# Performance work log

Measured on AMD Instinct MI355X. Metric: run time of the kernel, lower is better.

## Reference

```python
import jax, jax.numpy as jnp
import numpy as np

B_SZ, L, D_MODEL = 2, 2048, 2048
INTER, HEADS, P, N, G, K = 4096, 64, 64, 128, 1, 4
CONV_DIM = INTER + 2 * G * N
EPS = 1e-5


def silu(x):
    return x * jax.nn.sigmoid(x)


def softplus_thresh(x, threshold=10.0):
    # matches source: where(x < thr, log(1+exp(x)), x)
    return jnp.where(x < threshold, jnp.log1p(jnp.exp(jnp.minimum(x, threshold))), x)


def setup_inputs() -> dict:
    key = jax.random.key(0)
    ks = jax.random.split(key, 8)
    s = 0.02
    return {
        "hidden_states": jax.random.normal(ks[0], (B_SZ, L, D_MODEL), jnp.float32),
        "W_z": jax.random.normal(ks[1], (D_MODEL, INTER), jnp.float32) * s,
        "W_xBC": jax.random.normal(ks[2], (D_MODEL, CONV_DIM), jnp.float32) * s,
        "W_dt": jax.random.normal(ks[3], (D_MODEL, HEADS), jnp.float32) * s,
        "conv_w": jax.random.normal(ks[4], (CONV_DIM, K), jnp.float32) * 0.1,
        "conv_b": jnp.zeros((CONV_DIM,), jnp.float32),
        "dt_bias": jax.random.uniform(ks[5], (HEADS,), jnp.float32, -2.0, 0.0),
        "A_log": jnp.log(jnp.arange(1, HEADS + 1, dtype=jnp.float32)),
        "D": jnp.ones((HEADS,), jnp.float32),
        "norm_w": jnp.ones((INTER,), jnp.float32),
        "W_out": jax.random.normal(ks[6], (INTER, D_MODEL), jnp.float32) * s,
    }


def reference(hidden_states, W_z, W_xBC, W_dt, conv_w, conv_b, dt_bias, A_log, D, norm_w, W_out):
    b, l, _ = hidden_states.shape
    Hg = HEADS // G  # heads per group

    gate = hidden_states @ W_z                      # [b,l,INTER]
    xBC = hidden_states @ W_xBC                     # [b,l,CONV_DIM]
    dt = softplus_thresh(hidden_states @ W_dt + dt_bias)  # [b,l,H]

    # causal depthwise conv1d + silu (padding=K-1, truncated to seq_len)
    xp = jnp.pad(xBC, ((0, 0), (K - 1, 0), (0, 0)))
    kern = jnp.transpose(conv_w)[:, None, :]        # [K,1,CONV_DIM] (WIO)
    xBC = jax.lax.conv_general_dilated(
        xp, kern, (1,), 'VALID',
        dimension_numbers=('NWC', 'WIO', 'NWC'),
        feature_group_count=CONV_DIM)
    xBC = silu(xBC + conv_b)

    gns = G * N
    x = xBC[..., :INTER].reshape(b, l, G, Hg, P)
    Bm = xBC[..., INTER:INTER + gns].reshape(b, l, G, N)
    Cm = xBC[..., INTER + gns:].reshape(b, l, G, N)

    A = -jnp.exp(A_log)                             # [H]
    dA = jnp.exp(dt * A).reshape(b, l, G, Hg)       # [b,l,G,Hg]
    dtx = dt.reshape(b, l, G, Hg)[..., None] * x    # [b,l,G,Hg,P]

    def step(state, inp):
        dA_t, dtx_t, B_t, C_t = inp
        # state: [b,G,Hg,P,N]
        state = state * dA_t[..., None, None] + dtx_t[..., None] * B_t[:, :, None, None, :]
        y_t = jnp.einsum('bghpn,bgn->bghp', state, C_t)
        return state, y_t

    xs = (jnp.moveaxis(dA, 1, 0), jnp.moveaxis(dtx, 1, 0),
          jnp.moveaxis(Bm, 1, 0), jnp.moveaxis(Cm, 1, 0))
    state0 = jnp.zeros((b, G, Hg, P, N), jnp.float32)
    _, ys = jax.lax.scan(step, state0, xs)          # [l,b,G,Hg,P]
    y = jnp.moveaxis(ys, 0, 1) + D.reshape(G, Hg)[..., None] * x
    scan_out = y.reshape(b, l, INTER)

    # gated RMSNorm within groups
    hs = scan_out.reshape(b, l, G, INTER // G).astype(jnp.float32)
    gt = gate.reshape(b, l, G, INTER // G).astype(jnp.float32)
    hs = hs * silu(gt)
    var = jnp.mean(hs * hs, axis=-1, keepdims=True)
    hs = hs * jax.lax.rsqrt(var + EPS)
    normed = norm_w * hs.reshape(b, l, INTER)

    return normed @ W_out
```

## Files before the change

kernel.cpp:

```cpp
#include <hip/hip_runtime.h>
#include <hip/hip_bf16.h>
#include <math.h>

typedef unsigned short u16;
typedef unsigned int   u32;
typedef __attribute__((ext_vector_type(8))) short short8;
typedef __attribute__((ext_vector_type(4))) float f32x4;

#define B_SZ     2
#define LSEQ     2048
#define DMODEL   2048
#define INTER    4096
#define HEADS    64
#define NSTATE   128
#define CONV_DIM 4352
#define XCOLS    4480
#define EPS      1e-5f
#define QCH      64
#define NCHUNK   (LSEQ / QCH)

__device__ __forceinline__ float bf2f(u16 u) {
    u32 v = ((u32)u) << 16;
    return __builtin_bit_cast(float, v);
}
__device__ __forceinline__ u16 f2bf(float x) {
    __hip_bfloat16 h = __float2bfloat16(x);
    return __builtin_bit_cast(u16, h);
}
__device__ __forceinline__ u32 pack2(float lo, float hi) {
    return (u32)f2bf(lo) | ((u32)f2bf(hi) << 16);
}
__device__ __forceinline__ void gl2lds16(const void* g, void* l) {
    __builtin_amdgcn_global_load_lds(
        (const __attribute__((address_space(1))) u32*)g,
        (__attribute__((address_space(3))) u32*)l, 16, 0, 0);
}

__global__ __launch_bounds__(256) void cvt_f32_bf16(
    const float* __restrict__ in, u16* __restrict__ out, int n4)
{
    int i = blockIdx.x * 256 + threadIdx.x;
    if (i >= n4) return;
    float4 v = ((const float4*)in)[i];
    ushort4 o;
    o.x = f2bf(v.x); o.y = f2bf(v.y); o.z = f2bf(v.z); o.w = f2bf(v.w);
    ((ushort4*)out)[i] = o;
}

__global__ __launch_bounds__(256) void tr_f32_bf16(
    const float* __restrict__ in, u16* __restrict__ out, int R, int C)
{
    __shared__ u16 tile[64][68];
    const int r0 = blockIdx.y * 64, c0 = blockIdx.x * 64;
    const int tr = threadIdx.x >> 4, tc = (threadIdx.x & 15) * 4;
    #pragma unroll
    for (int i = 0; i < 4; ++i) {
        int r = tr + i * 16;
        float4 v = *(const float4*)(in + (size_t)(r0 + r) * C + c0 + tc);
        tile[r][tc + 0] = f2bf(v.x);
        tile[r][tc + 1] = f2bf(v.y);
        tile[r][tc + 2] = f2bf(v.z);
        tile[r][tc + 3] = f2bf(v.w);
    }
    __syncthreads();
    #pragma unroll
    for (int i = 0; i < 4; ++i) {
        int oc = tr + i * 16;
        ushort4 o;
        o.x = tile[tc + 0][oc];
        o.y = tile[tc + 1][oc];
        o.z = tile[tc + 2][oc];
        o.w = tile[tc + 3][oc];
        *(ushort4*)(out + (size_t)(c0 + oc) * R + r0 + tc) = o;
    }
}

template<int OUT_BF16>
__global__ __launch_bounds__(256) void gemm_nt(
    const u16* __restrict__ A, const u16* __restrict__ Bt,
    void* __restrict__ Co, int M, int N, int K)
{
    __shared__ __align__(16) u16 As[128 * 32];
    __shared__ __align__(16) u16 Bs[128 * 32];
    const int tid  = threadIdx.x;
    const int wave = tid >> 6, lane = tid & 63;
    const int m0 = blockIdx.y * 128, n0 = blockIdx.x * 128;
    const int wm = (wave >> 1) * 64, wn = (wave & 1) * 64;

    const int srow = wave * 16 + (lane >> 2);
    const int scol = (lane & 3) * 8;
    const u16* ag = A  + (size_t)(m0 + srow) * K + scol;
    const u16* bg = Bt + (size_t)(n0 + srow) * K + scol;
    u16* asl = As + wave * (16 * 32);
    u16* bsl = Bs + wave * (16 * 32);

    f32x4 acc[4][4];
    #pragma unroll
    for (int i = 0; i < 4; ++i)
        #pragma unroll
        for (int j = 0; j < 4; ++j) acc[i][j] = (f32x4)0.f;

    const int lr = lane & 15, lq = lane >> 4;
    const u16* arp = As + (wm + lr) * 32 + lq * 8;
    const u16* brp = Bs + (wn + lr) * 32 + lq * 8;

    for (int k0 = 0; k0 < K; k0 += 32) {
        __syncthreads();
        gl2lds16(ag + k0,          asl);
        gl2lds16(ag + 64 * K + k0, asl + 64 * 32);
        gl2lds16(bg + k0,          bsl);
        gl2lds16(bg + 64 * K + k0, bsl + 64 * 32);
        __syncthreads();

        short8 af[4], bfr[4];
        #pragma unroll
        for (int i = 0; i < 4; ++i) af[i]  = *(const short8*)(arp + i * 16 * 32);
        #pragma unroll
        for (int j = 0; j < 4; ++j) bfr[j] = *(const short8*)(brp + j * 16 * 32);
        #pragma unroll
        for (int i = 0; i < 4; ++i)
            #pragma unroll
            for (int j = 0; j < 4; ++j)
                acc[i][j] = __builtin_amdgcn_mfma_f32_16x16x32_bf16(
                    af[i], bfr[j], acc[i][j], 0, 0, 0);
    }

    #pragma unroll
    for (int i = 0; i < 4; ++i)
        #pragma unroll
        for (int j = 0; j < 4; ++j)
            #pragma unroll
            for (int r = 0; r < 4; ++r) {
                int row = m0 + wm + i * 16 + lq * 4 + r;
                int col = n0 + wn + j * 16 + lr;
                if (OUT_BF16)
                    ((u16*)Co)[(size_t)row * N + col] = f2bf(acc[i][j][r]);
                else
                    ((float*)Co)[(size_t)row * N + col] = acc[i][j][r];
            }
}

__global__ void dt_kernel(const u16* __restrict__ xpre,
                          float* __restrict__ dtb,
                          const float* __restrict__ dt_bias, int n)
{
    int i = blockIdx.x * 256 + threadIdx.x;
    if (i >= n) return;
    int h = i & 63, row = i >> 6;
    float x = bf2f(xpre[(size_t)row * XCOLS + CONV_DIM + h]) + dt_bias[h];
    dtb[i] = (x < 10.f) ? log1pf(expf(x)) : x;
}

__global__ void conv_kernel(const u16* __restrict__ xin,
                            const float* __restrict__ cw,
                            const float* __restrict__ cb,
                            u16* __restrict__ xout)
{
    int c  = blockIdx.x * 256 + threadIdx.x;
    int bt = blockIdx.y;
    int t  = bt & (LSEQ - 1);
    const u16* xi = xin + (size_t)bt * XCOLS + c;
    float4 w = *(const float4*)(cw + (size_t)c * 4);
    float acc = cb[c];
    acc = fmaf(bf2f(xi[0]), w.w, acc);
    if (t >= 1) acc = fmaf(bf2f(*(xi - XCOLS)),     w.z, acc);
    if (t >= 2) acc = fmaf(bf2f(*(xi - 2 * XCOLS)), w.y, acc);
    if (t >= 3) acc = fmaf(bf2f(*(xi - 3 * XCOLS)), w.x, acc);
    xout[(size_t)bt * CONV_DIM + c] = f2bf(acc / (1.f + expf(-acc)));
}

__global__ __launch_bounds__(256) void ssd_chunk_state(
    const u16* __restrict__ xc, const float* __restrict__ dtb,
    const float* __restrict__ A_log,
    u16* __restrict__ Tg, float* __restrict__ decayQ)
{
    const int bid = blockIdx.x;
    const int b = bid >> 11, h = (bid >> 5) & 63, c = bid & 31;
    const int t0 = c * QCH;
    const int tid = threadIdx.x;
    const int wave = tid >> 6, lane = tid & 63;
    const int lr = lane & 15, lq = lane >> 4;

    __shared__ __align__(16) u16 BT[128][72];
    __shared__ __align__(16) u16 XwT[64][72];
    __shared__ float sclL[QCH];

    const u16* xg = xc + (size_t)b * LSEQ * CONV_DIM;

    if (tid < 64) {
        float dtv = dtb[((size_t)b * LSEQ + t0 + tid) * HEADS + h];
        float a = -dtv * expf(A_log[h]);
        float s = a;
        #pragma unroll
        for (int off = 1; off < 64; off <<= 1) {
            float o = __shfl_up(s, off, 64);
            if (tid >= off) s += o;
        }
        float cq = __shfl(s, 63, 64);
        sclL[tid] = dtv * expf(cq - s);
        if (tid == 0) decayQ[((b * 64 + h) << 5) + c] = expf(cq);
    }
    __syncthreads();

    #pragma unroll
    for (int r = 0; r < 16; ++r) {
        int idx = tid + 256 * r, j = idx >> 6, p = idx & 63;
        float v = bf2f(xg[(size_t)(t0 + j) * CONV_DIM + h * 64 + p]);
        XwT[p][j] = f2bf(v * sclL[j]);
    }
    #pragma unroll
    for (int r = 0; r < 32; ++r) {
        int idx = tid + 256 * r, j = idx >> 7, n = idx & 127;
        BT[n][j] = xg[(size_t)(t0 + j) * CONV_DIM + INTER + n];
    }
    __syncthreads();

    f32x4 acc[8];
    #pragma unroll
    for (int i = 0; i < 8; ++i) acc[i] = (f32x4)0.f;
    #pragma unroll
    for (int k0 = 0; k0 < QCH; k0 += 32) {
        short8 af = *(const short8*)&XwT[wave * 16 + lr][k0 + lq * 8];
        #pragma unroll
        for (int nt = 0; nt < 8; ++nt) {
            short8 bfr = *(const short8*)&BT[nt * 16 + lr][k0 + lq * 8];
            acc[nt] = __builtin_amdgcn_mfma_f32_16x16x32_bf16(af, bfr, acc[nt], 0, 0, 0);
        }
    }
    u16* To = Tg + ((((size_t)(b * 64 + h)) * NCHUNK + c) * 64) * 128;
    #pragma unroll
    for (int nt = 0; nt < 8; ++nt)
        #pragma unroll
        for (int r = 0; r < 4; ++r)
            To[(wave * 16 + lq * 4 + r) * 128 + nt * 16 + lr] = f2bf(acc[nt][r]);
}

__global__ __launch_bounds__(256) void ssd_state_scan(
    u16* __restrict__ Tg, const float* __restrict__ decayQ)
{
    const int bh = blockIdx.x, tid = threadIdx.x;
    const int p = tid >> 2, nb = (tid & 3) * 32;
    float S[32];
    #pragma unroll
    for (int m = 0; m < 32; ++m) S[m] = 0.f;

    for (int c = 0; c < NCHUNK; ++c) {
        u16* base = Tg + ((((size_t)bh * NCHUNK + c) * 64 + p) * 128) + nb;
        uint4 tv[4];
        #pragma unroll
        for (int k = 0; k < 4; ++k) tv[k] = *(const uint4*)(base + k * 8);
        #pragma unroll
        for (int k = 0; k < 4; ++k) {
            uint4 sv;
            sv.x = pack2(S[k*8+0], S[k*8+1]);
            sv.y = pack2(S[k*8+2], S[k*8+3]);
            sv.z = pack2(S[k*8+4], S[k*8+5]);
            sv.w = pack2(S[k*8+6], S[k*8+7]);
            *(uint4*)(base + k * 8) = sv;
        }
        float dq = decayQ[(bh << 5) + c];
        #pragma unroll
        for (int k = 0; k < 4; ++k) {
            const u32* w = (const u32*)&tv[k];
            #pragma unroll
            for (int e = 0; e < 4; ++e) {
                S[k*8 + e*2]     = fmaf(dq, S[k*8 + e*2],     bf2f((u16)(w[e] & 0xffffu)));
                S[k*8 + e*2 + 1] = fmaf(dq, S[k*8 + e*2 + 1], bf2f((u16)(w[e] >> 16)));
            }
        }
    }
}

__global__ __launch_bounds__(256) void ssd_output(
    const u16* __restrict__ xc, const float* __restrict__ dtb,
    const float* __restrict__ A_log, const float* __restrict__ Dvec,
    const u16* __restrict__ Sg,
    u16* __restrict__ y)
{
    const int bid = blockIdx.x;
    const int b = bid >> 11, h = (bid >> 5) & 63, c = bid & 31;
    const int t0 = c * QCH;
    const int tid = threadIdx.x;
    const int wave = tid >> 6, lane = tid & 63;
    const int lr = lane & 15, lq = lane >> 4;

    __shared__ __align__(16) u16 C_lds[64][136];
    __shared__ __align__(16) u16 B_lds[64][136];
    __shared__ __align__(16) u16 S_lds[64][136];
    __shared__ __align__(16) u16 P_lds[64][72];
    __shared__ __align__(16) u16 XT[64][72];
    __shared__ float cumL[QCH], dtsL[QCH], escL[QCH];

    const u16* xg = xc + (size_t)b * LSEQ * CONV_DIM;

    if (tid < 64) {
        float dtv = dtb[((size_t)b * LSEQ + t0 + tid) * HEADS + h];
        float a = -dtv * expf(A_log[h]);
        float s = a;
        #pragma unroll
        for (int off = 1; off < 64; off <<= 1) {
            float o = __shfl_up(s, off, 64);
            if (tid >= off) s += o;
        }
        cumL[tid] = s;
        dtsL[tid] = dtv;
        escL[tid] = expf(s);
    }
    #pragma unroll
    for (int r4 = 0; r4 < 4; ++r4) {
        int idx4 = tid + 256 * r4;
        int j = idx4 >> 4, c8 = (idx4 & 15) * 8;
        *(uint4*)&B_lds[j][c8] = *(const uint4*)(xg + (size_t)(t0 + j) * CONV_DIM + INTER + c8);
        *(uint4*)&C_lds[j][c8] = *(const uint4*)(xg + (size_t)(t0 + j) * CONV_DIM + INTER + NSTATE + c8);
        *(uint4*)&S_lds[j][c8] = *(const uint4*)(Sg + ((((size_t)(b * 64 + h)) * NCHUNK + c) * 64 + j) * 128 + c8);
    }
    #pragma unroll
    for (int r = 0; r < 16; ++r) {
        int idx = tid + 256 * r, j = idx >> 6, p = idx & 63;
        XT[p][j] = xg[(size_t)(t0 + j) * CONV_DIM + h * 64 + p];
    }
    __syncthreads();

    f32x4 accG[4];
    #pragma unroll
    for (int i = 0; i < 4; ++i) accG[i] = (f32x4)0.f;
    #pragma unroll
    for (int k0 = 0; k0 < NSTATE; k0 += 32) {
        short8 af = *(const short8*)&C_lds[wave * 16 + lr][k0 + lq * 8];
        #pragma unroll
        for (int jt = 0; jt < 4; ++jt) {
            short8 bfr = *(const short8*)&B_lds[jt * 16 + lr][k0 + lq * 8];
            accG[jt] = __builtin_amdgcn_mfma_f32_16x16x32_bf16(af, bfr, accG[jt], 0, 0, 0);
        }
    }
    #pragma unroll
    for (int jt = 0; jt < 4; ++jt)
        #pragma unroll
        for (int r = 0; r < 4; ++r) {
            int ii = wave * 16 + lq * 4 + r;
            int jj = jt * 16 + lr;
            float v = (jj <= ii)
                ? accG[jt][r] * dtsL[jj] * expf(cumL[ii] - cumL[jj]) : 0.f;
            P_lds[ii][jj] = f2bf(v);
        }
    __syncthreads();

    f32x4 accY[4], accZ[4];
    #pragma unroll
    for (int i = 0; i < 4; ++i) { accY[i] = (f32x4)0.f; accZ[i] = (f32x4)0.f; }
    #pragma unroll
    for (int k0 = 0; k0 < QCH; k0 += 32) {
        short8 af = *(const short8*)&P_lds[wave * 16 + lr][k0 + lq * 8];
        #pragma unroll
        for (int pt = 0; pt < 4; ++pt) {
            short8 bfr = *(const short8*)&XT[pt * 16 + lr][k0 + lq * 8];
            accY[pt] = __builtin_amdgcn_mfma_f32_16x16x32_bf16(af, bfr, accY[pt], 0, 0, 0);
        }
    }
    #pragma unroll
    for (int k0 = 0; k0 < NSTATE; k0 += 32) {
        short8 af = *(const short8*)&C_lds[wave * 16 + lr][k0 + lq * 8];
        #pragma unroll
        for (int pt = 0; pt < 4; ++pt) {
            short8 bfr = *(const short8*)&S_lds[pt * 16 + lr][k0 + lq * 8];
            accZ[pt] = __builtin_amdgcn_mfma_f32_16x16x32_bf16(af, bfr, accZ[pt], 0, 0, 0);
        }
    }

    const float Dh = Dvec[h];
    u16* yg = y + ((size_t)b * LSEQ + t0) * INTER + h * 64;
    #pragma unroll
    for (int pt = 0; pt < 4; ++pt)
        #pragma unroll
        for (int r = 0; r < 4; ++r) {
            int ii = wave * 16 + lq * 4 + r;
            int pp = pt * 16 + lr;
            float xv = bf2f(XT[pp][ii]);
            float o = accY[pt][r] + escL[ii] * accZ[pt][r] + Dh * xv;
            yg[(size_t)ii * INTER + pp] = f2bf(o);
        }
}

__global__ __launch_bounds__(256) void norm_kernel(
    const u16* __restrict__ y, u16* __restrict__ gate,
    const float* __restrict__ w)
{
    const int row = blockIdx.x;
    const u16* yr = y    + (size_t)row * INTER;
    u16*       gr = gate + (size_t)row * INTER;
    const int tid = threadIdx.x;

    float v[16];
    float ss = 0.f;
    #pragma unroll
    for (int i = 0; i < 16; ++i) {
        int idx = tid + i * 256;
        float hv = bf2f(yr[idx]);
        float g  = bf2f(gr[idx]);
        float val = hv * (g / (1.f + expf(-g)));
        v[i] = val;
        ss = fmaf(val, val, ss);
    }
    #pragma unroll
    for (int o = 32; o > 0; o >>= 1) ss += __shfl_xor(ss, o);
    __shared__ float part[4];
    if ((tid & 63) == 0) part[tid >> 6] = ss;
    __syncthreads();
    float tot  = part[0] + part[1] + part[2] + part[3];
    float rinv = rsqrtf(tot * (1.f / INTER) + EPS);
    #pragma unroll
    for (int i = 0; i < 16; ++i) {
        int idx = tid + i * 256;
        gr[idx] = f2bf(w[idx] * v[i] * rinv);
    }
}

extern "C" void kernel_launch(void* const* d_in, const int* in_sizes, int n_in,
                              void* d_out, int out_size, void* d_ws, size_t ws_size,
                              hipStream_t stream)
{
    const float* hs      = (const float*)d_in[0];
    const float* W_z     = (const float*)d_in[1];
    const float* W_xBC   = (const float*)d_in[2];
    const float* W_dt    = (const float*)d_in[3];
    const float* conv_w  = (const float*)d_in[4];
    const float* conv_b  = (const float*)d_in[5];
    const float* dt_bias = (const float*)d_in[6];
    const float* A_log   = (const float*)d_in[7];
    const float* Dv      = (const float*)d_in[8];
    const float* norm_w  = (const float*)d_in[9];
    const float* W_out   = (const float*)d_in[10];
    float* out = (float*)d_out;
    char*  w8  = (char*)d_ws;

    u16* hs_bf  = (u16*)(w8 + 0);
    u16* Wt_z   = (u16*)(w8 + 16777216);
    u16* Wt_xc  = (u16*)(w8 + 33554432);
    u16* Tbuf   = (u16*)(w8 + 0);
    u16* Wt_out = (u16*)(w8 + 67108864);
    u16* gate   = (u16*)(w8 + 83886080);
    u16* xpre   = (u16*)(w8 + 117440512);
    u16* xconv  = (u16*)(w8 + 154140672);
    float* dtb  = (float*)(w8 + 189792256);
    float* dcq  = (float*)(w8 + 190840832);
    u16* yb = xpre;

    const int M = B_SZ * LSEQ;

    cvt_f32_bf16<<<(M * DMODEL / 4 + 255) / 256, 256, 0, stream>>>(hs, hs_bf, M * DMODEL / 4);
    tr_f32_bf16<<<dim3(INTER / 64,    DMODEL / 64), 256, 0, stream>>>(W_z,   Wt_z,  DMODEL, INTER);
    tr_f32_bf16<<<dim3(CONV_DIM / 64, DMODEL / 64), 256, 0, stream>>>(W_xBC, Wt_xc, DMODEL, CONV_DIM);
    tr_f32_bf16<<<dim3(1,             DMODEL / 64), 256, 0, stream>>>(W_dt,  Wt_xc + (size_t)CONV_DIM * DMODEL, DMODEL, 64);
    hipMemsetAsync(Wt_xc + (size_t)(CONV_DIM + 64) * DMODEL, 0, (size_t)64 * DMODEL * 2, stream);
    tr_f32_bf16<<<dim3(DMODEL / 64,   INTER / 64),  256, 0, stream>>>(W_out, Wt_out, INTER, DMODEL);

    gemm_nt<1><<<dim3(INTER / 128, M / 128), 256, 0, stream>>>(hs_bf, Wt_z,  (void*)gate, M, INTER, DMODEL);
    gemm_nt<1><<<dim3(XCOLS / 128, M / 128), 256, 0, stream>>>(hs_bf, Wt_xc, (void*)xpre, M, XCOLS, DMODEL);

    dt_kernel<<<(M * HEADS + 255) / 256, 256, 0, stream>>>(xpre, dtb, dt_bias, M * HEADS);
    conv_kernel<<<dim3(CONV_DIM / 256, M), 256, 0, stream>>>(xpre, conv_w, conv_b, xconv);

    ssd_chunk_state<<<B_SZ * HEADS * NCHUNK, 256, 0, stream>>>(xconv, dtb, A_log, Tbuf, dcq);
    ssd_state_scan<<<B_SZ * HEADS, 256, 0, stream>>>(Tbuf, dcq);
    ssd_output<<<B_SZ * HEADS * NCHUNK, 256, 0, stream>>>(xconv, dtb, A_log, Dv, Tbuf, yb);

    norm_kernel<<<M, 256, 0, stream>>>(yb, gate, norm_w);

    gemm_nt<0><<<dim3(DMODEL / 128, M / 128), 256, 0, stream>>>(gate, Wt_out, (void*)out, M, DMODEL, INTER);
}
```

Measured before the change: 699.9 us.

## Fuse z/xBC/dt projections into one GEMM and widen GEMM K-tile with swizzled LDS

Concatenates the transposed W_z, W_xBC and W_dt weights into one matrix so a single GEMM writes gate, xBC and dt into a shared strided buffer, removing one launch and re-reads of the activations. The GEMM K-step doubles to 64 with an XOR-swizzled LDS layout to reduce bank conflicts and halve barrier count. The epilogue uses lane shuffles to write paired columns as wider stores. Downstream kernels are re-pointed at the strided buffer, with y overwriting the xBC region in place.

```diff
diff --git a/kernel.cpp b/kernel.cpp
--- a/kernel.cpp
+++ b/kernel.cpp
@@ -14,7 +14,8 @@
 #define HEADS    64
 #define NSTATE   128
 #define CONV_DIM 4352
-#define XCOLS    4480
+#define XSTR     8576
+#define NFUSE    8576
 #define EPS      1e-5f
 #define QCH      64
 #define NCHUNK   (LSEQ / QCH)
@@ -78,21 +79,18 @@
 template<int OUT_BF16>
 __global__ __launch_bounds__(256) void gemm_nt(
     const u16* __restrict__ A, const u16* __restrict__ Bt,
-    void* __restrict__ Co, int M, int N, int K)
-{
-    __shared__ __align__(16) u16 As[128 * 32];
-    __shared__ __align__(16) u16 Bs[128 * 32];
+    void* __restrict__ Co, int M, int N, int K, int lda)
+{
+    __shared__ __align__(16) u16 As[128 * 64];
+    __shared__ __align__(16) u16 Bs[128 * 64];
     const int tid  = threadIdx.x;
     const int wave = tid >> 6, lane = tid & 63;
     const int m0 = blockIdx.y * 128, n0 = blockIdx.x * 128;
     const int wm = (wave >> 1) * 64, wn = (wave & 1) * 64;
 
-    const int srow = wave * 16 + (lane >> 2);
-    const int scol = (lane & 3) * 8;
-    const u16* ag = A  + (size_t)(m0 + srow) * K + scol;
-    const u16* bg = Bt + (size_t)(n0 + srow) * K + scol;
-    u16* asl = As + wave * (16 * 32);
-    u16* bsl = Bs + wave * (16 * 32);
+    const int l3  = lane >> 3, lcb = lane & 7;
+    const int swrow = wave * 32;
+    const int scb8  = (lcb ^ l3) << 3;
 
     f32x4 acc[4][4];
     #pragma unroll
@@ -101,57 +99,78 @@
         for (int j = 0; j < 4; ++j) acc[i][j] = (f32x4)0.f;
 
     const int lr = lane & 15, lq = lane >> 4;
-    const u16* arp = As + (wm + lr) * 32 + lq * 8;
-    const u16* brp = Bs + (wn + lr) * 32 + lq * 8;
-
-    for (int k0 = 0; k0 < K; k0 += 32) {
+
+    for (int k0 = 0; k0 < K; k0 += 64) {
         __syncthreads();
-        gl2lds16(ag + k0,          asl);
-        gl2lds16(ag + 64 * K + k0, asl + 64 * 32);
-        gl2lds16(bg + k0,          bsl);
-        gl2lds16(bg + 64 * K + k0, bsl + 64 * 32);
+        #pragma unroll
+        for (int q = 0; q < 4; ++q) {
+            int row = swrow + q * 8 + l3;
+            gl2lds16(A  + (size_t)(m0 + row) * lda + scb8 + k0, As + (swrow + q * 8) * 64);
+            gl2lds16(Bt + (size_t)(n0 + row) * K   + scb8 + k0, Bs + (swrow + q * 8) * 64);
+        }
         __syncthreads();
 
-        short8 af[4], bfr[4];
-        #pragma unroll
-        for (int i = 0; i < 4; ++i) af[i]  = *(const short8*)(arp + i * 16 * 32);
-        #pragma unroll
-        for (int j = 0; j < 4; ++j) bfr[j] = *(const short8*)(brp + j * 16 * 32);
-        #pragma unroll
-        for (int i = 0; i < 4; ++i)
+        #pragma unroll
+        for (int kk = 0; kk < 2; ++kk) {
+            short8 af[4], bfr[4];
             #pragma unroll
-            for (int j = 0; j < 4; ++j)
-                acc[i][j] = __builtin_amdgcn_mfma_f32_16x16x32_bf16(
-                    af[i], bfr[j], acc[i][j], 0, 0, 0);
-    }
-
+            for (int i = 0; i < 4; ++i) {
+                int row = wm + i * 16 + lr;
+                int slot = (kk * 4 + lq) ^ (lr & 7);
+                af[i] = *(const short8*)(As + row * 64 + slot * 8);
+            }
+            #pragma unroll
+            for (int j = 0; j < 4; ++j) {
+                int row = wn + j * 16 + lr;
+                int slot = (kk * 4 + lq) ^ (lr & 7);
+                bfr[j] = *(const short8*)(Bs + row * 64 + slot * 8);
+            }
+            #pragma unroll
+            for (int i = 0; i < 4; ++i)
+                #pragma unroll
+                for (int j = 0; j < 4; ++j)
+                    acc[i][j] = __builtin_amdgcn_mfma_f32_16x16x32_bf16(
+                        af[i], bfr[j], acc[i][j], 0, 0, 0);
+        }
+    }
+
+    const int odd  = lr & 1;
     #pragma unroll
     for (int i = 0; i < 4; ++i)
         #pragma unroll
-        for (int j = 0; j < 4; ++j)
-            #pragma unroll
-            for (int r = 0; r < 4; ++r) {
-                int row = m0 + wm + i * 16 + lq * 4 + r;
-                int col = n0 + wn + j * 16 + lr;
-                if (OUT_BF16)
-                    ((u16*)Co)[(size_t)row * N + col] = f2bf(acc[i][j][r]);
-                else
-                    ((float*)Co)[(size_t)row * N + col] = acc[i][j][r];
+        for (int j = 0; j < 4; ++j) {
+            float v0 = acc[i][j][0], v1 = acc[i][j][1];
+            float v2 = acc[i][j][2], v3 = acc[i][j][3];
+            float n0v = __shfl_xor(v0, 1), n1v = __shfl_xor(v1, 1);
+            float n2v = __shfl_xor(v2, 1), n3v = __shfl_xor(v3, 1);
+            int colb  = n0 + wn + j * 16 + (lr & ~1);
+            int rbase = m0 + wm + i * 16 + lq * 4 + odd * 2;
+            if (OUT_BF16) {
+                u32 w0 = odd ? pack2(n2v, v2) : pack2(v0, n0v);
+                u32 w1 = odd ? pack2(n3v, v3) : pack2(v1, n1v);
+                *(u32*)((u16*)Co + (size_t)rbase * N + colb) = w0;
+                *(u32*)((u16*)Co + (size_t)(rbase + 1) * N + colb) = w1;
+            } else {
+                float2 f0 = odd ? make_float2(n2v, v2) : make_float2(v0, n0v);
+                float2 f1 = odd ? make_float2(n3v, v3) : make_float2(v1, n1v);
+                *(float2*)((float*)Co + (size_t)rbase * N + colb) = f0;
+                *(float2*)((float*)Co + (size_t)(rbase + 1) * N + colb) = f1;
             }
-}
-
-__global__ void dt_kernel(const u16* __restrict__ xpre,
+        }
+}
+
+__global__ void dt_kernel(const u16* __restrict__ xall,
                           float* __restrict__ dtb,
                           const float* __restrict__ dt_bias, int n)
 {
     int i = blockIdx.x * 256 + threadIdx.x;
     if (i >= n) return;
     int h = i & 63, row = i >> 6;
-    float x = bf2f(xpre[(size_t)row * XCOLS + CONV_DIM + h]) + dt_bias[h];
+    float x = bf2f(xall[(size_t)row * XSTR + INTER + CONV_DIM + h]) + dt_bias[h];
     dtb[i] = (x < 10.f) ? log1pf(expf(x)) : x;
 }
 
-__global__ void conv_kernel(const u16* __restrict__ xin,
+__global__ void conv_kernel(const u16* __restrict__ xall,
                             const float* __restrict__ cw,
                             const float* __restrict__ cb,
                             u16* __restrict__ xout)
@@ -159,13 +178,13 @@
     int c  = blockIdx.x * 256 + threadIdx.x;
     int bt = blockIdx.y;
     int t  = bt & (LSEQ - 1);
-    const u16* xi = xin + (size_t)bt * XCOLS + c;
+    const u16* xi = xall + (size_t)bt * XSTR + INTER + c;
     float4 w = *(const float4*)(cw + (size_t)c * 4);
     float acc = cb[c];
     acc = fmaf(bf2f(xi[0]), w.w, acc);
-    if (t >= 1) acc = fmaf(bf2f(*(xi - XCOLS)),     w.z, acc);
-    if (t >= 2) acc = fmaf(bf2f(*(xi - 2 * XCOLS)), w.y, acc);
-    if (t >= 3) acc = fmaf(bf2f(*(xi - 3 * XCOLS)), w.x, acc);
+    if (t >= 1) acc = fmaf(bf2f(*(xi - XSTR)),     w.z, acc);
+    if (t >= 2) acc = fmaf(bf2f(*(xi - 2 * XSTR)), w.y, acc);
+    if (t >= 3) acc = fmaf(bf2f(*(xi - 3 * XSTR)), w.x, acc);
     xout[(size_t)bt * CONV_DIM + c] = f2bf(acc / (1.f + expf(-acc)));
 }
 
@@ -368,7 +387,7 @@
     }
 
     const float Dh = Dvec[h];
-    u16* yg = y + ((size_t)b * LSEQ + t0) * INTER + h * 64;
+    u16* yg = y + ((size_t)b * LSEQ + t0) * XSTR + h * 64;
     #pragma unroll
     for (int pt = 0; pt < 4; ++pt)
         #pragma unroll
@@ -377,17 +396,16 @@
             int pp = pt * 16 + lr;
             float xv = bf2f(XT[pp][ii]);
             float o = accY[pt][r] + escL[ii] * accZ[pt][r] + Dh * xv;
-            yg[(size_t)ii * INTER + pp] = f2bf(o);
+            yg[(size_t)ii * XSTR + pp] = f2bf(o);
         }
 }
 
 __global__ __launch_bounds__(256) void norm_kernel(
-    const u16* __restrict__ y, u16* __restrict__ gate,
-    const float* __restrict__ w)
+    u16* __restrict__ xall, const float* __restrict__ w)
 {
     const int row = blockIdx.x;
-    const u16* yr = y    + (size_t)row * INTER;
-    u16*       gr = gate + (size_t)row * INTER;
+    const u16* yr = xall + (size_t)row * XSTR + INTER;
+    u16*       gr = xall + (size_t)row * XSTR;
     const int tid = threadIdx.x;
 
     float v[16];
@@ -434,37 +452,35 @@
     char*  w8  = (char*)d_ws;
 
     u16* hs_bf  = (u16*)(w8 + 0);
-    u16* Wt_z   = (u16*)(w8 + 16777216);
-    u16* Wt_xc  = (u16*)(w8 + 33554432);
+    u16* Wt_all = (u16*)(w8 + 16777216);
     u16* Tbuf   = (u16*)(w8 + 0);
     u16* Wt_out = (u16*)(w8 + 67108864);
-    u16* gate   = (u16*)(w8 + 83886080);
-    u16* xpre   = (u16*)(w8 + 117440512);
+    u16* xall   = (u16*)(w8 + 83886080);
     u16* xconv  = (u16*)(w8 + 154140672);
     float* dtb  = (float*)(w8 + 189792256);
     float* dcq  = (float*)(w8 + 190840832);
-    u16* yb = xpre;
 
     const int M = B_SZ * LSEQ;
 
     cvt_f32_bf16<<<(M * DMODEL / 4 + 255) / 256, 256, 0, stream>>>(hs, hs_bf, M * DMODEL / 4);
-    tr_f32_bf16<<<dim3(INTER / 64,    DMODEL / 64), 256, 0, stream>>>(W_z,   Wt_z,  DMODEL, INTER);
-    tr_f32_bf16<<<dim3(CONV_DIM / 64, DMODEL / 64), 256, 0, stream>>>(W_xBC, Wt_xc, DMODEL, CONV_DIM);
-    tr_f32_bf16<<<dim3(1,             DMODEL / 64), 256, 0, stream>>>(W_dt,  Wt_xc + (size_t)CONV_DIM * DMODEL, DMODEL, 64);
-    hipMemsetAsync(Wt_xc + (size_t)(CONV_DIM + 64) * DMODEL, 0, (size_t)64 * DMODEL * 2, stream);
+    tr_f32_bf16<<<dim3(INTER / 64,    DMODEL / 64), 256, 0, stream>>>(W_z,   Wt_all, DMODEL, INTER);
+    tr_f32_bf16<<<dim3(CONV_DIM / 64, DMODEL / 64), 256, 0, stream>>>(W_xBC, Wt_all + (size_t)INTER * DMODEL, DMODEL, CONV_DIM);
+    tr_f32_bf16<<<dim3(1,             DMODEL / 64), 256, 0, stream>>>(W_dt,  Wt_all + (size_t)(INTER + CONV_DIM) * DMODEL, DMODEL, 64);
+    hipMemsetAsync(Wt_all + (size_t)(INTER + CONV_DIM + 64) * DMODEL, 0, (size_t)64 * DMODEL * 2, stream);
     tr_f32_bf16<<<dim3(DMODEL / 64,   INTER / 64),  256, 0, stream>>>(W_out, Wt_out, INTER, DMODEL);
 
-    gemm_nt<1><<<dim3(INTER / 128, M / 128), 256, 0, stream>>>(hs_bf, Wt_z,  (void*)gate, M, INTER, DMODEL);
-    gemm_nt<1><<<dim3(XCOLS / 128, M / 128), 256, 0, stream>>>(hs_bf, Wt_xc, (void*)xpre, M, XCOLS, DMODEL);
-
-    dt_kernel<<<(M * HEADS + 255) / 256, 256, 0, stream>>>(xpre, dtb, dt_bias, M * HEADS);
-    conv_kernel<<<dim3(CONV_DIM / 256, M), 256, 0, stream>>>(xpre, conv_w, conv_b, xconv);
+    gemm_nt<1><<<dim3(NFUSE / 128, M / 128), 256, 0, stream>>>(
+        hs_bf, Wt_all, (void*)xall, M, NFUSE, DMODEL, DMODEL);
+
+    dt_kernel<<<(M * HEADS + 255) / 256, 256, 0, stream>>>(xall, dtb, dt_bias, M * HEADS);
+    conv_kernel<<<dim3(CONV_DIM / 256, M), 256, 0, stream>>>(xall, conv_w, conv_b, xconv);
 
     ssd_chunk_state<<<B_SZ * HEADS * NCHUNK, 256, 0, stream>>>(xconv, dtb, A_log, Tbuf, dcq);
     ssd_state_scan<<<B_SZ * HEADS, 256, 0, stream>>>(Tbuf, dcq);
-    ssd_output<<<B_SZ * HEADS * NCHUNK, 256, 0, stream>>>(xconv, dtb, A_log, Dv, Tbuf, yb);
-
-    norm_kernel<<<M, 256, 0, stream>>>(yb, gate, norm_w);
-
-    gemm_nt<0><<<dim3(DMODEL / 128, M / 128), 256, 0, stream>>>(gate, Wt_out, (void*)out, M, DMODEL, INTER);
-}
+    ssd_output<<<B_SZ * HEADS * NCHUNK, 256, 0, stream>>>(xconv, dtb, A_log, Dv, Tbuf, xall + INTER);
+
+    norm_kernel<<<M, 256, 0, stream>>>(xall, norm_w);
+
+    gemm_nt<0><<<dim3(DMODEL / 128, M / 128), 256, 0, stream>>>(
+        xall, Wt_out, (void*)out, M, DMODEL, INTER, XSTR);
+}
```

Result: faster. 632.3 us (-9.7%).
